# Optimization experiments

Hardware: AMD Instinct MI355X
Metric: run time of the kernel (lower is better)

## Reference

```python
import jax, jax.numpy as jnp
import numpy as np

BETA = 0.5
OT_ITER = 50
OT_K = 1
EPS = 1e-5


def _l2norm(x, eps=EPS):
    n = jnp.linalg.norm(x, axis=-1, keepdims=True)
    return x / jnp.maximum(n, eps)


def cost_matrix_cosine(x, y):
    # [B,M,D],[B,N,D] -> [B,M,N] cosine distance
    return 1.0 - jnp.einsum('bmd,bnd->bmn', _l2norm(x), _l2norm(y))


def ipot(C, x_len, x_pad, y_pad, y_len, joint_pad, beta, iteration, k):
    # C: [B,M,N] (already detached). Returns transport plan T: [B,N,M].
    b, m, n = C.shape
    jp_t = jnp.swapaxes(joint_pad, 1, 2)                      # [B,N,M]
    sigma = jnp.where(x_pad, 0.0, 1.0 / x_len[:, None])       # [B,M]
    sigma = sigma[:, :, None]                                 # [B,M,1]
    T = jnp.where(jp_t, 0.0, 1.0).astype(C.dtype)             # [B,N,M]
    A = jnp.where(jp_t, 0.0, jnp.exp(-jnp.swapaxes(C, 1, 2) / beta))
    x_mask = (x_pad.astype(C.dtype) * 1e4)[:, None, :]        # [B,1,M]
    y_mask = (y_pad.astype(C.dtype) * 1e4)[:, None, :]        # [B,1,N]
    xl = x_len[:, None, None]
    yl = y_len[:, None, None]

    def outer(carry, _):
        T, sigma = carry
        Q = A * T                                             # [B,N,M]

        def inner(sig, _):
            # sig: [B,M,1]
            delta = 1.0 / (yl * jnp.swapaxes(Q @ sig, 1, 2) + y_mask)   # [B,1,N]
            sig_new = 1.0 / (xl * (delta @ Q) + x_mask)                 # [B,1,M]
            return jnp.swapaxes(sig_new, 1, 2), delta

        sigma, deltas = jax.lax.scan(inner, sigma, None, length=k)
        delta = deltas[-1]                                    # [B,1,N]
        T_new = jnp.swapaxes(delta, 1, 2) * Q * jnp.swapaxes(sigma, 1, 2)
        return (T_new, sigma), None

    (T, _), _ = jax.lax.scan(outer, (T, sigma), None, length=iteration)
    return jnp.where(jp_t, 0.0, T)


def optimal_transport_dist(txt_emb, img_emb, txt_pad, img_pad,
                           beta=BETA, iteration=OT_ITER, k=OT_K):
    cost = cost_matrix_cosine(txt_emb, img_emb)               # [B,M,N]
    joint_pad = txt_pad[:, :, None] | img_pad[:, None, :]
    cost = jnp.where(joint_pad, 0.0, cost)
    txt_len = (txt_pad.shape[1] - txt_pad.sum(1)).astype(cost.dtype)
    img_len = (img_pad.shape[1] - img_pad.sum(1)).astype(cost.dtype)
    T = ipot(jax.lax.stop_gradient(cost), txt_len, txt_pad, img_pad,
             img_len, joint_pad, beta, iteration, k)
    T = jax.lax.stop_gradient(T)
    # trace(cost @ T)  == einsum over matching indices
    return jnp.einsum('bmn,bnm->b', cost, T)


def crf_llh(emissions, tags, mask, start_transitions, end_transitions, transitions):
    # emissions [T,B,K], tags [T,B] int, mask [T,B] bool (mask[0] all True)
    T, B, K = emissions.shape
    b_idx = jnp.arange(B)
    maskf = mask.astype(emissions.dtype)

    # numerator: gold path score
    score = start_transitions[tags[0]] + emissions[0, b_idx, tags[0]]
    trans_sc = transitions[tags[:-1], tags[1:]] * maskf[1:]              # [T-1,B]
    emit_sc = jnp.take_along_axis(emissions[1:], tags[1:][..., None], axis=-1)[..., 0] * maskf[1:]
    score = score + trans_sc.sum(0) + emit_sc.sum(0)
    seq_ends = mask.astype(jnp.int32).sum(0) - 1
    last_tags = tags[seq_ends, b_idx]
    numerator = score + end_transitions[last_tags]

    # denominator: forward algorithm (log-sum-exp recurrence)
    def step(s, inp):
        emis_t, mask_t = inp
        nxt = jax.nn.logsumexp(s[:, :, None] + transitions[None] + emis_t[:, None, :], axis=1)
        return jnp.where(mask_t[:, None], nxt, s), None

    init = start_transitions[None, :] + emissions[0]                     # [B,K]
    final, _ = jax.lax.scan(step, init, (emissions[1:], mask[1:]))
    denominator = jax.nn.logsumexp(final + end_transitions[None, :], axis=1)
    return numerator - denominator                                       # [B]


def setup_inputs() -> dict:
    key = jax.random.key(0)
    ks = jax.random.split(key, 10)
    T, B, K = 512, 64, 21
    M, N, D = 512, 512, 768

    emissions = jax.random.normal(ks[0], (T, B, K), dtype=jnp.float32)
    txt_emb = jax.random.normal(ks[1], (B, M, D), dtype=jnp.float32)
    img_emb = jax.random.normal(ks[2], (B, N, D), dtype=jnp.float32)

    start_transitions = jax.random.uniform(ks[3], (K,), minval=-0.1, maxval=0.1)
    end_transitions = jax.random.uniform(ks[4], (K,), minval=-0.1, maxval=0.1)
    transitions = jax.random.uniform(ks[5], (K, K), minval=-0.1, maxval=0.1)

    tags = jax.random.randint(ks[6], (T, B), 0, K)
    crf_len = jax.random.randint(ks[7], (B,), T // 2, T + 1)
    crf_mask = jnp.arange(T)[:, None] < crf_len[None, :]   # mask[0] all True
    txt_len = jax.random.randint(ks[8], (B,), M // 2, M + 1)
    txt_pad = jnp.arange(M)[None, :] >= txt_len[:, None]
    img_len = jax.random.randint(ks[9], (B,), N // 2, N + 1)
    img_pad = jnp.arange(N)[None, :] >= img_len[:, None]

    return {
        'emissions': emissions, 'txt_emb': txt_emb, 'img_emb': img_emb,
        'start_transitions': start_transitions, 'end_transitions': end_transitions,
        'transitions': transitions, 'tags': tags, 'crf_mask': crf_mask,
        'txt_pad': txt_pad, 'img_pad': img_pad,
    }


def reference(emissions, txt_emb, img_emb, start_transitions, end_transitions,
              transitions, tags, crf_mask, txt_pad, img_pad):
    llh = crf_llh(emissions, tags, crf_mask, start_transitions,
                  end_transitions, transitions)              # [B]
    ot = optimal_transport_dist(txt_emb, img_emb, txt_pad, img_pad)  # [B]
    loss = -llh.sum() + ot.sum()
    return loss
```

## Files before the change

kernel.cpp:

```cpp
#include <hip/hip_runtime.h>
#include <stdint.h>

typedef unsigned short u16;
typedef unsigned char u8;
typedef unsigned int u32;

#define LOG2E 1.4426950408889634f
#define LN2   0.6931471805599453f

typedef __attribute__((ext_vector_type(2))) float f32x2;

__device__ __forceinline__ float exp2_(float x){ return __builtin_amdgcn_exp2f(x); }
__device__ __forceinline__ float log2_(float x){ return __builtin_amdgcn_logf(x); }
__device__ __forceinline__ float bflo(u32 u){ return __uint_as_float(u << 16); }
__device__ __forceinline__ float bfhi(u32 u){ return __uint_as_float(u & 0xffff0000u); }
__device__ __forceinline__ u16 f2bf(float f){
  u32 u = __float_as_uint(f);
  return (u16)((u + 0x7fffu + ((u >> 16) & 1u)) >> 16);
}
__device__ __forceinline__ u32 pkbf(float lo, float hi){
  u32 r; asm("v_cvt_pk_bf16_f32 %0, %1, %2" : "=v"(r) : "v"(lo), "v"(hi)); return r;
}
__device__ __forceinline__ int rdmask(const u8* p, int i, int st){ return (int)p[(size_t)i * st]; }

__global__ void k_detect(const u32* __restrict__ cmask, int* __restrict__ flags) {
  flags[0] = (cmask[0] == 0x01010101u) ? 1 : 4;
}

__global__ __launch_bounds__(256) void k_normalize(const float* __restrict__ txt,
                                                   const float* __restrict__ img,
                                                   u16* __restrict__ xh, u16* __restrict__ yh) {
  int row = blockIdx.x * 4 + (threadIdx.x >> 6);
  int l = threadIdx.x & 63;
  const float* src; u16* dst;
  if (row < 32768) { src = txt + (size_t)row * 768; dst = xh + (size_t)row * 768; }
  else { int r2 = row - 32768; src = img + (size_t)r2 * 768; dst = yh + (size_t)r2 * 768; }
  float v[12]; float ss = 0.f;
  #pragma unroll
  for (int s = 0; s < 12; ++s) { v[s] = src[l + (s << 6)]; ss = fmaf(v[s], v[s], ss); }
  #pragma unroll
  for (int off = 32; off; off >>= 1) ss += __shfl_xor(ss, off);
  float sc = 1.0f / fmaxf(sqrtf(ss), 1e-5f);
  #pragma unroll
  for (int s = 0; s < 12; ++s) dst[l + (s << 6)] = f2bf(v[s] * sc);
}

typedef __attribute__((ext_vector_type(8))) short short8;
typedef __attribute__((ext_vector_type(4))) float f32x4;

__global__ __launch_bounds__(256) void k_gemm_crf(const u16* __restrict__ xh, const u16* __restrict__ yh,
                                                  const u8* __restrict__ xpad, const u8* __restrict__ ypad,
                                                  const int* __restrict__ flags,
                                                  u16* __restrict__ Ct2,
                                                  const float* __restrict__ emis, const int* __restrict__ tags,
                                                  const u8* __restrict__ mask,
                                                  const float* __restrict__ startT, const float* __restrict__ endT,
                                                  const float* __restrict__ trans, float* __restrict__ llh) {
  __shared__ u16 As[128 * 64];
  __shared__ u16 Bs[128 * 64];
  __shared__ float tr[441];
  int st = flags[0];
  int bt = blockIdx.x;
  int tid = threadIdx.x;

  if (bt >= 1024) {
    int b = bt - 1024;
    for (int i = tid; i < 441; i += 256) tr[i] = trans[i];
    __syncthreads();
    if (tid >= 64) return;
    int k = tid;
    float accs = 0.f; int cnt = 0;
    for (int t = k; t < 512; t += 64) {
      int mt = rdmask(mask, (t << 6) + b, st);
      cnt += mt;
      int tg = tags[(t << 6) + b];
      if (t == 0) {
        accs += startT[tg] + emis[(size_t)b * 21 + tg];
      } else if (mt) {
        int tgp = tags[((t - 1) << 6) + b];
        accs += tr[tgp * 21 + tg] + emis[((size_t)((t << 6) + b)) * 21 + tg];
      }
    }
    #pragma unroll
    for (int off = 32; off; off >>= 1) { accs += __shfl_down(accs, off); cnt += __shfl_down(cnt, off); }
    float numer = 0.f;
    if (k == 0) {
      int last = tags[((cnt - 1) << 6) + b];
      numer = accs + endT[last];
    }
    int kc = (k < 21) ? k : 20;
    float s = startT[kc] + emis[(size_t)b * 21 + kc];
    for (int t = 1; t < 512; ++t) {
      float z[21];
      float zmax = -3.0e38f;
      #pragma unroll
      for (int j = 0; j < 21; ++j) {
        float sj = __shfl(s, j);
        z[j] = sj + tr[j * 21 + kc];
        zmax = fmaxf(zmax, z[j]);
      }
      float sum = 0.f;
      #pragma unroll
      for (int j = 0; j < 21; ++j) sum += exp2_((z[j] - zmax) * LOG2E);
      float ns = zmax + log2_(sum) * LN2 + emis[((size_t)((t << 6) + b)) * 21 + kc];
      s = rdmask(mask, (t << 6) + b, st) ? ns : s;
    }
    float f = (k < 21) ? (s + endT[kc]) : -3.0e38f;
    float m = f;
    #pragma unroll
    for (int off = 32; off; off >>= 1) m = fmaxf(m, __shfl_xor(m, off));
    float sum = (k < 21) ? exp2_((f - m) * LOG2E) : 0.f;
    #pragma unroll
    for (int off = 32; off; off >>= 1) sum += __shfl_xor(sum, off);
    float denom = m + log2_(sum) * LN2;
    if (k == 0) llh[b] = numer - denom;
    return;
  }

  int b = bt >> 4;
  int tile = bt & 15;
  int tn = tile >> 2, tm = tile & 3;
  const u16* Ab = yh + ((size_t)b * 512 + tn * 128) * 768;
  const u16* Bb = xh + ((size_t)b * 512 + tm * 128) * 768;
  int w = tid >> 6, l = tid & 63;
  int wr = (w >> 1) << 6, wc = (w & 1) << 6;
  f32x4 acc[4][4] = {};
  for (int k0 = 0; k0 < 768; k0 += 64) {
    #pragma unroll
    for (int q = 0; q < 4; ++q) {
      int slot = (q << 8) + tid;
      int row = slot >> 3, col = (slot & 7) << 3;
      uint4 va = *(const uint4*)(Ab + row * 768 + k0 + col);
      uint4 vb = *(const uint4*)(Bb + row * 768 + k0 + col);
      *(uint4*)((char*)As + slot * 16) = va;
      *(uint4*)((char*)Bs + slot * 16) = vb;
    }
    __syncthreads();
    #pragma unroll
    for (int kk = 0; kk < 64; kk += 32) {
      int cb = (kk + ((l >> 4) << 3)) * 2;
      short8 a[4], bb[4];
      #pragma unroll
      for (int i = 0; i < 4; ++i)
        a[i] = *(const short8*)((const char*)As + (wr + (i << 4) + (l & 15)) * 128 + cb);
      #pragma unroll
      for (int j = 0; j < 4; ++j)
        bb[j] = *(const short8*)((const char*)Bs + (wc + (j << 4) + (l & 15)) * 128 + cb);
      #pragma unroll
      for (int i = 0; i < 4; ++i)
        #pragma unroll
        for (int j = 0; j < 4; ++j)
          acc[i][j] = __builtin_amdgcn_mfma_f32_16x16x32_bf16(a[i], bb[j], acc[i][j], 0, 0, 0);
    }
    __syncthreads();
  }
  int n0 = (tn << 7) + wr, m0 = (tm << 7) + wc;
  #pragma unroll
  for (int i = 0; i < 4; ++i) {
    #pragma unroll
    for (int j = 0; j < 4; ++j) {
      int m = m0 + (j << 4) + (l & 15);
      int xpm = rdmask(xpad, b * 512 + m, st);
      #pragma unroll
      for (int r = 0; r < 4; ++r) {
        int n = n0 + (i << 4) + ((l >> 4) << 2) + r;
        float v = 2.8853901f * (1.0f - acc[i][j][r]);
        if (xpm | rdmask(ypad, b * 512 + n, st)) v = 30000.0f;
        Ct2[((size_t)(b * 512 + n) << 9) + m] = f2bf(v);
      }
    }
  }
}

__device__ __forceinline__ void batch_barrier(int* cnt, int target) {
  __syncthreads();
  if (threadIdx.x == 0) {
    __hip_atomic_fetch_add(cnt, 1, __ATOMIC_RELEASE, __HIP_MEMORY_SCOPE_AGENT);
    while (__hip_atomic_load(cnt, __ATOMIC_ACQUIRE, __HIP_MEMORY_SCOPE_AGENT) < target)
      __builtin_amdgcn_s_sleep(1);
  }
  __syncthreads();
}

__global__ __launch_bounds__(1024)
void k_ipot_f8b(const u16* __restrict__ Ct2,
                const u8* __restrict__ xpad, const u8* __restrict__ ypad,
                const int* __restrict__ flags,
                int* __restrict__ gcount, float* __restrict__ c_part,
                float* __restrict__ fin_part,
                float* __restrict__ ot) {
  __shared__ __align__(16) u32  A_l[128 * 128];
  __shared__ __align__(16) float cpart[16][512];
  __shared__ __align__(16) float sig[512];
  __shared__ __align__(16) float xmk[512];
  __shared__ __align__(16) float ymk[512];
  __shared__ float redw[16];
  __shared__ int cnti[2];

  int bid = blockIdx.x;
  int b = bid & 63, p = bid >> 6;
  int tid = threadIdx.x;
  int w = tid >> 6, l = tid & 63;
  int st = flags[0];

  if (tid < 2) cnti[tid] = 0;
  __syncthreads();
  if (tid < 512) {
    int xp = rdmask(xpad, (b << 9) + tid, st) ? 1 : 0;
    int yp = rdmask(ypad, (b << 9) + tid, st) ? 1 : 0;
    xmk[tid] = xp ? 1e4f : 0.f;
    ymk[tid] = yp ? 1e4f : 0.f;
    atomicAdd(&cnti[0], 1 - xp);
    atomicAdd(&cnti[1], 1 - yp);
  }
  __syncthreads();
  float xl = (float)cnti[0], yl = (float)cnti[1];
  if (tid < 512) sig[tid] = (xmk[tid] > 0.f) ? 0.f : (1.0f / xl);

  const int base_n = p << 7;
  const int row0 = (w << 3);
  const u16* Cb = Ct2 + ((size_t)(b * 512 + base_n) << 9);
  int* cnt_b = gcount + (b << 6);
  float* cp_b = c_part + ((size_t)b << 12);

  u32 Tp[32];
  #pragma unroll
  for (int r = 0; r < 8; ++r) {
    const uint4 cv = *(const uint4*)(Cb + (size_t)(row0 + r) * 512 + (l << 3));
    float a0 = exp2_(-bflo(cv.x)), a1 = exp2_(-bfhi(cv.x));
    float a2 = exp2_(-bflo(cv.y)), a3 = exp2_(-bfhi(cv.y));
    float a4 = exp2_(-bflo(cv.z)), a5 = exp2_(-bfhi(cv.z));
    float a6 = exp2_(-bflo(cv.w)), a7 = exp2_(-bfhi(cv.w));
    u32 w0 = (u32)__builtin_amdgcn_cvt_pk_fp8_f32(a0, a1, 0, false);
    w0 = (u32)__builtin_amdgcn_cvt_pk_fp8_f32(a2, a3, (int)w0, true);
    u32 w1 = (u32)__builtin_amdgcn_cvt_pk_fp8_f32(a4, a5, 0, false);
    w1 = (u32)__builtin_amdgcn_cvt_pk_fp8_f32(a6, a7, (int)w1, true);
    uint2 wv; wv.x = w0; wv.y = w1;
    *(uint2*)(A_l + (row0 + r) * 128 + (l << 1)) = wv;
    Tp[r * 4 + 0] = 0x3F803F80u;
    Tp[r * 4 + 1] = 0x3F803F80u;
    Tp[r * 4 + 2] = 0x3F803F80u;
    Tp[r * 4 + 3] = 0x3F803F80u;
  }
  __syncthreads();

  const int k0b = l & 1, k1b = (l >> 1) & 1, k2b = (l >> 2) & 1;
  const int myr = (k0b << 2) | (k1b << 1) | k2b;
  const float ymk_mine_base = 0.f; (void)ymk_mine_base;

  for (int it = 1; it <= 50; ++it) {
    int par = it & 1;
    float dl[8];
    {
      float sg[8];
      const float4* ps = (const float4*)&sig[l << 3];
      float4 s0v = ps[0], s1v = ps[1];
      sg[0]=s0v.x; sg[1]=s0v.y; sg[2]=s0v.z; sg[3]=s0v.w;
      sg[4]=s1v.x; sg[5]=s1v.y; sg[6]=s1v.z; sg[7]=s1v.w;
      float rp[8];
      #pragma unroll
      for (int r = 0; r < 8; ++r) {
        const uint2 av = *(const uint2*)(A_l + (row0 + r) * 128 + (l << 1));
        f32x2 a01 = __builtin_amdgcn_cvt_pk_f32_fp8((int)av.x, false);
        f32x2 a23 = __builtin_amdgcn_cvt_pk_f32_fp8((int)av.x, true);
        f32x2 a45 = __builtin_amdgcn_cvt_pk_f32_fp8((int)av.y, false);
        f32x2 a67 = __builtin_amdgcn_cvt_pk_f32_fp8((int)av.y, true);
        float acc = 0.f;
        { u32 tw = Tp[r*4+0]; float q0 = a01.x*bflo(tw), q1 = a01.y*bfhi(tw);
          Tp[r*4+0] = pkbf(q0,q1); acc = fmaf(q0,sg[0],acc); acc = fmaf(q1,sg[1],acc); }
        { u32 tw = Tp[r*4+1]; float q0 = a23.x*bflo(tw), q1 = a23.y*bfhi(tw);
          Tp[r*4+1] = pkbf(q0,q1); acc = fmaf(q0,sg[2],acc); acc = fmaf(q1,sg[3],acc); }
        { u32 tw = Tp[r*4+2]; float q0 = a45.x*bflo(tw), q1 = a45.y*bfhi(tw);
          Tp[r*4+2] = pkbf(q0,q1); acc = fmaf(q0,sg[4],acc); acc = fmaf(q1,sg[5],acc); }
        { u32 tw = Tp[r*4+3]; float q0 = a67.x*bflo(tw), q1 = a67.y*bfhi(tw);
          Tp[r*4+3] = pkbf(q0,q1); acc = fmaf(q0,sg[6],acc); acc = fmaf(q1,sg[7],acc); }
        rp[r] = acc;
      }
      float s0 = (k0b ? rp[4] : rp[0]) + __shfl_xor(k0b ? rp[0] : rp[4], 1);
      float s1 = (k0b ? rp[5] : rp[1]) + __shfl_xor(k0b ? rp[1] : rp[5], 1);
      float s2 = (k0b ? rp[6] : rp[2]) + __shfl_xor(k0b ? rp[2] : rp[6], 1);
      float s3 = (k0b ? rp[7] : rp[3]) + __shfl_xor(k0b ? rp[3] : rp[7], 1);
      float t0 = (k1b ? s2 : s0) + __shfl_xor(k1b ? s0 : s2, 2);
      float t1 = (k1b ? s3 : s1) + __shfl_xor(k1b ? s1 : s3, 2);
      float u0 = (k2b ? t1 : t0) + __shfl_xor(k2b ? t0 : t1, 4);
      u0 += __shfl_xor(u0, 8);
      u0 += __shfl_xor(u0, 16);
      u0 += __shfl_xor(u0, 32);
      float dmine = 1.0f / fmaf(yl, u0, ymk[base_n + row0 + myr]);
      #pragma unroll
      for (int r = 0; r < 8; ++r)
        dl[r] = __shfl(dmine, (((r & 1) << 2) | (r & 2) | ((r >> 2) & 1)));
    }
    {
      float cp[8] = {0.f,0.f,0.f,0.f,0.f,0.f,0.f,0.f};
      #pragma unroll
      for (int r = 0; r < 8; ++r) {
        float d = dl[r];
        { u32 tw = Tp[r*4+0]; cp[0] = fmaf(bflo(tw),d,cp[0]); cp[1] = fmaf(bfhi(tw),d,cp[1]); }
        { u32 tw = Tp[r*4+1]; cp[2] = fmaf(bflo(tw),d,cp[2]); cp[3] = fmaf(bfhi(tw),d,cp[3]); }
        { u32 tw = Tp[r*4+2]; cp[4] = fmaf(bflo(tw),d,cp[4]); cp[5] = fmaf(bfhi(tw),d,cp[5]); }
        { u32 tw = Tp[r*4+3]; cp[6] = fmaf(bflo(tw),d,cp[6]); cp[7] = fmaf(bfhi(tw),d,cp[7]); }
      }
      float4 v0, v1;
      v0.x=cp[0]; v0.y=cp[1]; v0.z=cp[2]; v0.w=cp[3];
      v1.x=cp[4]; v1.y=cp[5]; v1.z=cp[6]; v1.w=cp[7];
      float4* dst = (float4*)&cpart[w][l << 3];
      dst[0] = v0; dst[1] = v1;
      __syncthreads();
    }
    if (tid < 512) {
      float s = 0.f;
      #pragma unroll
      for (int k = 0; k < 16; ++k) s += cpart[k][tid];
      __hip_atomic_store(&cp_b[(par << 11) + (p << 9) + tid], s, __ATOMIC_RELAXED, __HIP_MEMORY_SCOPE_AGENT);
    }
    batch_barrier(&cnt_b[it - 1], 4);
    if (tid < 512) {
      const float* basep = cp_b + (par << 11);
      float s = __hip_atomic_load(&basep[tid], __ATOMIC_RELAXED, __HIP_MEMORY_SCOPE_AGENT);
      s += __hip_atomic_load(&basep[512 + tid], __ATOMIC_RELAXED, __HIP_MEMORY_SCOPE_AGENT);
      s += __hip_atomic_load(&basep[1024 + tid], __ATOMIC_RELAXED, __HIP_MEMORY_SCOPE_AGENT);
      s += __hip_atomic_load(&basep[1536 + tid], __ATOMIC_RELAXED, __HIP_MEMORY_SCOPE_AGENT);
      sig[tid] = 1.0f / fmaf(xl, s, xmk[tid]);
    }
    __syncthreads();
    {
      float sg[8];
      const float4* ps = (const float4*)&sig[l << 3];
      float4 s0v = ps[0], s1v = ps[1];
      sg[0]=s0v.x; sg[1]=s0v.y; sg[2]=s0v.z; sg[3]=s0v.w;
      sg[4]=s1v.x; sg[5]=s1v.y; sg[6]=s1v.z; sg[7]=s1v.w;
      #pragma unroll
      for (int r = 0; r < 8; ++r) {
        float d = dl[r];
        { u32 tw = Tp[r*4+0]; Tp[r*4+0] = pkbf(bflo(tw)*d*sg[0], bfhi(tw)*d*sg[1]); }
        { u32 tw = Tp[r*4+1]; Tp[r*4+1] = pkbf(bflo(tw)*d*sg[2], bfhi(tw)*d*sg[3]); }
        { u32 tw = Tp[r*4+2]; Tp[r*4+2] = pkbf(bflo(tw)*d*sg[4], bfhi(tw)*d*sg[5]); }
        { u32 tw = Tp[r*4+3]; Tp[r*4+3] = pkbf(bflo(tw)*d*sg[6], bfhi(tw)*d*sg[7]); }
      }
    }
  }

  float accT = 0.f;
  #pragma unroll
  for (int r = 0; r < 8; ++r) {
    const uint4 cv = *(const uint4*)(Cb + (size_t)(row0 + r) * 512 + (l << 3));
    { u32 tw = Tp[r*4+0]; accT = fmaf(bflo(cv.x), bflo(tw), accT); accT = fmaf(bfhi(cv.x), bfhi(tw), accT); }
    { u32 tw = Tp[r*4+1]; accT = fmaf(bflo(cv.y), bflo(tw), accT); accT = fmaf(bfhi(cv.y), bfhi(tw), accT); }
    { u32 tw = Tp[r*4+2]; accT = fmaf(bflo(cv.z), bflo(tw), accT); accT = fmaf(bfhi(cv.z), bfhi(tw), accT); }
    { u32 tw = Tp[r*4+3]; accT = fmaf(bflo(cv.w), bflo(tw), accT); accT = fmaf(bfhi(cv.w), bfhi(tw), accT); }
  }
  #pragma unroll
  for (int off = 32; off; off >>= 1) accT += __shfl_xor(accT, off);
  if (l == 0) redw[w] = accT;
  __syncthreads();
  if (tid == 0) {
    float s = 0.f;
    #pragma unroll
    for (int ww = 0; ww < 16; ++ww) s += redw[ww];
    __hip_atomic_store(&fin_part[(b << 2) + p], s, __ATOMIC_RELAXED, __HIP_MEMORY_SCOPE_AGENT);
  }
  batch_barrier(&cnt_b[50], 4);
  if (p == 0 && tid == 0) {
    float s = 0.f;
    #pragma unroll
    for (int pp = 0; pp < 4; ++pp)
      s += __hip_atomic_load(&fin_part[(b << 2) + pp], __ATOMIC_RELAXED, __HIP_MEMORY_SCOPE_AGENT);
    ot[b] = s * 0.34657359f;
  }
}

__global__ __launch_bounds__(64) void k_finalize(const float* __restrict__ llh, const float* __restrict__ ot,
                                                 float* __restrict__ out) {
  int l = threadIdx.x;
  float v = ot[l] - llh[l];
  #pragma unroll
  for (int off = 32; off; off >>= 1) v += __shfl_down(v, off);
  if (l == 0) out[0] = v;
}

extern "C" void kernel_launch(void* const* d_in, const int* in_sizes, int n_in,
                              void* d_out, int out_size, void* d_ws, size_t ws_size,
                              hipStream_t stream) {
  const float* emis  = (const float*)d_in[0];
  const float* txt   = (const float*)d_in[1];
  const float* img   = (const float*)d_in[2];
  const float* startT= (const float*)d_in[3];
  const float* endT  = (const float*)d_in[4];
  const float* trans = (const float*)d_in[5];
  const int*  tags   = (const int*)d_in[6];
  const u8* cmask = (const u8*)d_in[7];
  const u8* xpad  = (const u8*)d_in[8];
  const u8* ypad  = (const u8*)d_in[9];
  char* wsb = (char*)d_ws;
  u16* xh  = (u16*)wsb;
  u16* yh  = (u16*)(wsb + 50331648ll);
  u16* Ct2 = (u16*)(wsb + 100663296ll);
  float* ot    = (float*)(wsb + 134217728ll);
  float* llh   = ot + 64;
  int*  flags  = (int*)(llh + 64);
  int*  gcount = (int*)(wsb + 134218752ll);
  float* c_part= (float*)(wsb + 134235136ll);
  float* fin_part=(float*)(wsb + 135283712ll);
  float* out = (float*)d_out;

  hipMemsetAsync(gcount, 0, 64 * 64 * sizeof(int), stream);
  hipLaunchKernelGGL(k_detect, dim3(1), dim3(1), 0, stream, (const u32*)cmask, flags);
  hipLaunchKernelGGL(k_normalize, dim3(16384), dim3(256), 0, stream, txt, img, xh, yh);
  hipLaunchKernelGGL(k_gemm_crf, dim3(1088), dim3(256), 0, stream, xh, yh, xpad, ypad, flags, Ct2,
                     emis, tags, cmask, startT, endT, trans, llh);
  hipLaunchKernelGGL(k_ipot_f8b, dim3(256), dim3(1024), 0, stream,
                     Ct2, xpad, ypad, flags, gcount, c_part, fin_part, ot);
  hipLaunchKernelGGL(k_finalize, dim3(1), dim3(64), 0, stream, llh, ot, out);
}
```

Before: 741.8 us.

## Split IPOT per batch across eight 512-thread blocks instead of four 1024-thread blocks

```diff
diff --git a/kernel.cpp b/kernel.cpp
--- a/kernel.cpp
+++ b/kernel.cpp
@@ -182,30 +182,31 @@
   __syncthreads();
 }
 
-__global__ __launch_bounds__(1024)
-void k_ipot_f8b(const u16* __restrict__ Ct2,
-                const u8* __restrict__ xpad, const u8* __restrict__ ypad,
-                const int* __restrict__ flags,
-                int* __restrict__ gcount, float* __restrict__ c_part,
-                float* __restrict__ fin_part,
-                float* __restrict__ ot) {
-  __shared__ __align__(16) u32  A_l[128 * 128];
-  __shared__ __align__(16) float cpart[16][512];
+__global__ __launch_bounds__(512)
+void k_ipot512(const u16* __restrict__ Ct2,
+               const u8* __restrict__ xpad, const u8* __restrict__ ypad,
+               const int* __restrict__ flags,
+               int* __restrict__ gcount, float* __restrict__ c_part,
+               float* __restrict__ fin_part,
+               float* __restrict__ ot) {
+  __shared__ __align__(16) u32  A_l[64 * 128];
+  __shared__ __align__(16) float cpart[8][512];
   __shared__ __align__(16) float sig[512];
   __shared__ __align__(16) float xmk[512];
   __shared__ __align__(16) float ymk[512];
-  __shared__ float redw[16];
+  __shared__ float redw[8];
   __shared__ int cnti[2];
 
   int bid = blockIdx.x;
-  int b = bid & 63, p = bid >> 6;
+  int b = ((bid >> 6) << 3) | (bid & 7);
+  int p = (bid >> 3) & 7;
   int tid = threadIdx.x;
   int w = tid >> 6, l = tid & 63;
   int st = flags[0];
 
   if (tid < 2) cnti[tid] = 0;
   __syncthreads();
-  if (tid < 512) {
+  {
     int xp = rdmask(xpad, (b << 9) + tid, st) ? 1 : 0;
     int yp = rdmask(ypad, (b << 9) + tid, st) ? 1 : 0;
     xmk[tid] = xp ? 1e4f : 0.f;
@@ -215,13 +216,14 @@
   }
   __syncthreads();
   float xl = (float)cnti[0], yl = (float)cnti[1];
-  if (tid < 512) sig[tid] = (xmk[tid] > 0.f) ? 0.f : (1.0f / xl);
-
-  const int base_n = p << 7;
+  sig[tid] = (xmk[tid] > 0.f) ? 0.f : (1.0f / xl);
+  __syncthreads();
+
+  const int base_n = p << 6;
   const int row0 = (w << 3);
   const u16* Cb = Ct2 + ((size_t)(b * 512 + base_n) << 9);
   int* cnt_b = gcount + (b << 6);
-  float* cp_b = c_part + ((size_t)b << 12);
+  float* cp_b = c_part + (size_t)b * 8192;
 
   u32 Tp[32];
   #pragma unroll
@@ -246,7 +248,6 @@
 
   const int k0b = l & 1, k1b = (l >> 1) & 1, k2b = (l >> 2) & 1;
   const int myr = (k0b << 2) | (k1b << 1) | k2b;
-  const float ymk_mine_base = 0.f; (void)ymk_mine_base;
 
   for (int it = 1; it <= 50; ++it) {
     int par = it & 1;
@@ -308,19 +309,19 @@
       dst[0] = v0; dst[1] = v1;
       __syncthreads();
     }
-    if (tid < 512) {
+    {
       float s = 0.f;
       #pragma unroll
-      for (int k = 0; k < 16; ++k) s += cpart[k][tid];
-      __hip_atomic_store(&cp_b[(par << 11) + (p << 9) + tid], s, __ATOMIC_RELAXED, __HIP_MEMORY_SCOPE_AGENT);
-    }
-    batch_barrier(&cnt_b[it - 1], 4);
-    if (tid < 512) {
-      const float* basep = cp_b + (par << 11);
-      float s = __hip_atomic_load(&basep[tid], __ATOMIC_RELAXED, __HIP_MEMORY_SCOPE_AGENT);
-      s += __hip_atomic_load(&basep[512 + tid], __ATOMIC_RELAXED, __HIP_MEMORY_SCOPE_AGENT);
-      s += __hip_atomic_load(&basep[1024 + tid], __ATOMIC_RELAXED, __HIP_MEMORY_SCOPE_AGENT);
-      s += __hip_atomic_load(&basep[1536 + tid], __ATOMIC_RELAXED, __HIP_MEMORY_SCOPE_AGENT);
+      for (int k = 0; k < 8; ++k) s += cpart[k][tid];
+      __hip_atomic_store(&cp_b[(par << 12) + (p << 9) + tid], s, __ATOMIC_RELAXED, __HIP_MEMORY_SCOPE_AGENT);
+    }
+    batch_barrier(&cnt_b[it - 1], 8);
+    {
+      const float* basep = cp_b + (par << 12);
+      float s = 0.f;
+      #pragma unroll
+      for (int pp = 0; pp < 8; ++pp)
+        s += __hip_atomic_load(&basep[(pp << 9) + tid], __ATOMIC_RELAXED, __HIP_MEMORY_SCOPE_AGENT);
       sig[tid] = 1.0f / fmaf(xl, s, xmk[tid]);
     }
     __syncthreads();
@@ -357,15 +358,15 @@
   if (tid == 0) {
     float s = 0.f;
     #pragma unroll
-    for (int ww = 0; ww < 16; ++ww) s += redw[ww];
-    __hip_atomic_store(&fin_part[(b << 2) + p], s, __ATOMIC_RELAXED, __HIP_MEMORY_SCOPE_AGENT);
-  }
-  batch_barrier(&cnt_b[50], 4);
+    for (int ww = 0; ww < 8; ++ww) s += redw[ww];
+    __hip_atomic_store(&fin_part[(b << 3) + p], s, __ATOMIC_RELAXED, __HIP_MEMORY_SCOPE_AGENT);
+  }
+  batch_barrier(&cnt_b[50], 8);
   if (p == 0 && tid == 0) {
     float s = 0.f;
     #pragma unroll
-    for (int pp = 0; pp < 4; ++pp)
-      s += __hip_atomic_load(&fin_part[(b << 2) + pp], __ATOMIC_RELAXED, __HIP_MEMORY_SCOPE_AGENT);
+    for (int pp = 0; pp < 8; ++pp)
+      s += __hip_atomic_load(&fin_part[(b << 3) + pp], __ATOMIC_RELAXED, __HIP_MEMORY_SCOPE_AGENT);
     ot[b] = s * 0.34657359f;
   }
 }
@@ -399,17 +400,17 @@
   float* ot    = (float*)(wsb + 134217728ll);
   float* llh   = ot + 64;
   int*  flags  = (int*)(llh + 64);
-  int*  gcount = (int*)(wsb + 134218752ll);
-  float* c_part= (float*)(wsb + 134235136ll);
-  float* fin_part=(float*)(wsb + 135283712ll);
+  int*  gcount  = (int*)wsb;
+  float* c_part = (float*)(wsb + 16384ll);
+  float* fin_part=(float*)(wsb + 16384ll + 2097152ll);
   float* out = (float*)d_out;
 
-  hipMemsetAsync(gcount, 0, 64 * 64 * sizeof(int), stream);
   hipLaunchKernelGGL(k_detect, dim3(1), dim3(1), 0, stream, (const u32*)cmask, flags);
   hipLaunchKernelGGL(k_normalize, dim3(16384), dim3(256), 0, stream, txt, img, xh, yh);
   hipLaunchKernelGGL(k_gemm_crf, dim3(1088), dim3(256), 0, stream, xh, yh, xpad, ypad, flags, Ct2,
                      emis, tags, cmask, startT, endT, trans, llh);
-  hipLaunchKernelGGL(k_ipot_f8b, dim3(256), dim3(1024), 0, stream,
+  hipMemsetAsync(gcount, 0, 64 * 64 * sizeof(int), stream);
+  hipLaunchKernelGGL(k_ipot512, dim3(512), dim3(512), 0, stream,
                      Ct2, xpad, ypad, flags, gcount, c_part, fin_part, ot);
   hipLaunchKernelGGL(k_finalize, dim3(1), dim3(64), 0, stream, llh, ot, out);
 }
```

Result: slower. 1.004 ms (+35.4%).
